# Kernel tuning notes

Hardware: AMD Instinct MI355X
Metric: run time of the kernel (lower is better)

Reference implementation:

```python
import jax, jax.numpy as jnp
import numpy as np

LN2 = float(np.log(2.0))

def ssp(v):
    # PhysNet shifted softplus activation
    return jax.nn.softplus(v) - LN2

N, F, E, K, L = 50000, 128, 800000, 64, 3

def setup_inputs() -> dict:
    key = jax.random.key(0)
    ks = jax.random.split(key, 16)
    sc = 1.0 / np.sqrt(F)
    x = jax.random.normal(ks[0], (N, F), dtype=jnp.float32)
    rbf = jax.random.uniform(ks[1], (E, K), dtype=jnp.float32)
    idx_i = jnp.sort(jax.random.randint(ks[2], (E,), 0, N, dtype=jnp.int32))
    idx_j = jax.random.randint(ks[3], (E,), 0, N, dtype=jnp.int32)
    Wk2f = jax.random.normal(ks[4], (K, F), dtype=jnp.float32) / np.sqrt(K)
    Wi = jax.random.normal(ks[5], (F, F), dtype=jnp.float32) * sc
    bi = jnp.zeros((F,), jnp.float32)
    Wj = jax.random.normal(ks[6], (F, F), dtype=jnp.float32) * sc
    bj = jnp.zeros((F,), jnp.float32)
    Wr1 = jax.random.normal(ks[7], (L, F, F), dtype=jnp.float32) * sc
    br1 = jnp.zeros((L, F), jnp.float32)
    Wr2 = jax.random.normal(ks[8], (L, F, F), dtype=jnp.float32) * sc
    br2 = jnp.zeros((L, F), jnp.float32)
    Wf = jax.random.normal(ks[9], (F, F), dtype=jnp.float32) * sc
    bf = jnp.zeros((F,), jnp.float32)
    u = jnp.ones((F,), jnp.float32)
    return dict(x=x, rbf=rbf, Wk2f=Wk2f, Wi=Wi, bi=bi, Wj=Wj, bj=bj,
                Wr1=Wr1, br1=br1, Wr2=Wr2, br2=br2, Wf=Wf, bf=bf, u=u,
                idx_i=idx_i, idx_j=idx_j)

def reference(x, rbf, Wk2f, Wi, bi, Wj, bj, Wr1, br1, Wr2, br2, Wf, bf, u, idx_i, idx_j):
    xa = ssp(x)                                   # [N,F] (drop_rate=0 -> no dropout)
    g = rbf @ Wk2f                                # [E,F] rbf gate
    xi = ssp(xa @ Wi + bi)                        # [N,F]
    xj_all = ssp(xa @ Wj + bj)                    # [N,F]
    msgs = g * xj_all[idx_j]                      # [E,F] gather + gate
    xj = jax.ops.segment_sum(msgs, idx_i, num_segments=N)  # [N,F] scatter-reduce
    m = xi + xj
    for l in range(L):                            # PhysNet residual blocks
        y = ssp(m)
        m = m + ssp(y @ Wr1[l] + br1[l]) @ Wr2[l] + br2[l]
    m = ssp(m)
    return u * x + (m @ Wf + bf)
```

## Files before the change

### kernel.cpp

```cpp
#include <hip/hip_runtime.h>
#include <hip/hip_bf16.h>
#include <math.h>

typedef unsigned short u16;
typedef short bf16x8 __attribute__((ext_vector_type(8)));
typedef float f32x4 __attribute__((ext_vector_type(4)));

#define LN2F 0.693147180559945f

__device__ __forceinline__ float bf2f(u16 h) {
  union { unsigned int i; float f; } v; v.i = ((unsigned int)h) << 16; return v.f;
}
__device__ __forceinline__ u16 f2bf(float f) {
  union { float f; unsigned int i; } v; v.f = f;
  unsigned int x = v.i;
  return (u16)((x + 0x7fffu + ((x >> 16) & 1u)) >> 16);
}
__device__ __forceinline__ float sspf(float v) {
  return fmaxf(v, 0.0f) + __logf(1.0f + __expf(-fabsf(v))) - LN2F;
}
template<int MODE>
__device__ __forceinline__ float ldv(const void* p, size_t i) {
  if constexpr (MODE == 0) return bf2f(((const u16*)p)[i]);
  else                     return ((const float*)p)[i];
}

__global__ void probe_k(const u16* __restrict__ x, int* __restrict__ flag) {
  __shared__ int sf;
  if (threadIdx.x == 0) sf = 0;
  __syncthreads();
  int f = 0;
  for (int i = threadIdx.x; i < 4096; i += 256) {
    const unsigned e = (x[i] >> 7) & 0xFFu;
    if (e >= 0xC0u) f = 1;
  }
  if (f) atomicOr(&sf, 1);
  __syncthreads();
  if (threadIdx.x == 0) *flag = sf;
}

template<int NB>
__device__ __forceinline__ void copy_lin(const u16* __restrict__ g, u16* s, int tid) {
  constexpr int CH = NB / 16;
#pragma unroll
  for (int c = tid; c < CH; c += 256)
    *(bf16x8*)(s + (size_t)c * 8) = *(const bf16x8*)(g + (size_t)c * 8);
}

__device__ __forceinline__ void wload(const u16* __restrict__ g, bf16x8* w, int tid) {
#pragma unroll
  for (int p = 0; p < 8; ++p) w[p] = *(const bf16x8*)(g + (size_t)(tid + p * 256) * 8);
  if (tid < 128) w[8] = *(const bf16x8*)(g + (size_t)(2048 + tid) * 8);
}
__device__ __forceinline__ void wstore(u16* s, const bf16x8* w, int tid) {
#pragma unroll
  for (int p = 0; p < 8; ++p) *(bf16x8*)(s + (size_t)(tid + p * 256) * 8) = w[p];
  if (tid < 128) *(bf16x8*)(s + (size_t)(2048 + tid) * 8) = w[8];
}

template<int KSTEPS, int LDW>
__device__ __forceinline__ void mm_lds(const u16* sA, const u16* sW, f32x4* acc,
                                       int m16, int quad) {
#pragma unroll
  for (int s = 0; s < KSTEPS; ++s) {
    const int k0 = s * 32 + quad * 8;
    bf16x8 a = *(const bf16x8*)(sA + (size_t)m16 * LDW + k0);
#pragma unroll
    for (int t = 0; t < 8; ++t) {
      bf16x8 b = *(const bf16x8*)(sW + (size_t)(t * 16 + m16) * LDW + k0);
      acc[t] = __builtin_amdgcn_mfma_f32_16x16x32_bf16(a, b, acc[t], 0, 0, 0);
    }
  }
}

template<int MODE>
__global__ __launch_bounds__(256) void prep_k(
    const int* __restrict__ mode,
    const void* __restrict__ Wi, const void* __restrict__ Wj,
    const void* __restrict__ Wf, const void* __restrict__ Wk2f,
    const void* __restrict__ Wr1, const void* __restrict__ Wr2,
    u16* __restrict__ WT, int L)
{
  if (*mode != MODE) return;
  const int b = blockIdx.x, tid = threadIdx.x;
  constexpr size_t esz = (MODE == 0) ? 2 : 4;
  const void* src; u16* dst; int KD = 128, LDW = 136;
  if      (b == 0) { src = Wi;  dst = WT; }
  else if (b == 1) { src = Wj;  dst = WT + 17408; }
  else if (b == 2) { src = Wf;  dst = WT + 2 * 17408; }
  else if (b == 3) { src = Wk2f; dst = WT + (size_t)(3 + 2 * L) * 17408; KD = 64; LDW = 72; }
  else if (b < 4 + L) { int l = b - 4;     src = (const char*)Wr1 + (size_t)l * 16384 * esz; dst = WT + (size_t)(3 + l) * 17408; }
  else                { int l = b - 4 - L; src = (const char*)Wr2 + (size_t)l * 16384 * esz; dst = WT + (size_t)(3 + L + l) * 17408; }

  const int n  = tid & 127;
  const int kh = (tid >> 7) * (KD >> 1);
  for (int c = 0; c < (KD >> 4); ++c) {
    const int k0 = kh + c * 8;
    bf16x8 rv;
#pragma unroll
    for (int j = 0; j < 8; ++j)
      rv[j] = (short)f2bf(ldv<MODE>(src, (size_t)(k0 + j) * 128 + n));
    *(bf16x8*)(dst + (size_t)n * LDW + k0) = rv;
  }
}

template<int MODE>
__global__ __launch_bounds__(256) void in_k(
    const int* __restrict__ mode, const void* __restrict__ x,
    const u16* __restrict__ WiT, const u16* __restrict__ WjT,
    const void* __restrict__ bi, const void* __restrict__ bj,
    float* __restrict__ mb, u16* __restrict__ xjt, int N)
{
  if (*mode != MODE) return;
  __shared__ u16 sW[128 * 136];
  const int tid = threadIdx.x, lane = tid & 63, wave = tid >> 6;
  const int m16 = lane & 15, quad = lane >> 4;
  const int row_tile = blockIdx.x * 64 + wave * 16;
  int arow = row_tile + m16; if (arow >= N) arow = N - 1;

  bf16x8 af[4];
#pragma unroll
  for (int s = 0; s < 4; ++s) {
    const int k0 = s * 32 + quad * 8;
    if constexpr (MODE == 0) {
      bf16x8 raw = *(const bf16x8*)((const u16*)x + (size_t)arow * 128 + k0);
#pragma unroll
      for (int j = 0; j < 8; ++j) af[s][j] = (short)f2bf(sspf(bf2f((u16)raw[j])));
    } else {
      const float* ap = (const float*)x + (size_t)arow * 128 + k0;
      float4 lo = *(const float4*)ap, hi = *(const float4*)(ap + 4);
      float v[8] = {lo.x, lo.y, lo.z, lo.w, hi.x, hi.y, hi.z, hi.w};
#pragma unroll
      for (int j = 0; j < 8; ++j) af[s][j] = (short)f2bf(sspf(v[j]));
    }
  }

  copy_lin<128 * 136 * 2>(WiT, sW, tid);
  __syncthreads();
  f32x4 aI[8], aJ[8];
#pragma unroll
  for (int t = 0; t < 8; ++t) aI[t] = (f32x4){0.f, 0.f, 0.f, 0.f};
  bf16x8 w[9];
  wload(WjT, w, tid);
#pragma unroll
  for (int s = 0; s < 4; ++s) {
    const int k0 = s * 32 + quad * 8;
#pragma unroll
    for (int t = 0; t < 8; ++t) {
      bf16x8 b = *(const bf16x8*)(sW + (size_t)(t * 16 + m16) * 136 + k0);
      aI[t] = __builtin_amdgcn_mfma_f32_16x16x32_bf16(af[s], b, aI[t], 0, 0, 0);
    }
  }
  __syncthreads();
  wstore(sW, w, tid);
  __syncthreads();
#pragma unroll
  for (int t = 0; t < 8; ++t) aJ[t] = (f32x4){0.f, 0.f, 0.f, 0.f};
#pragma unroll
  for (int s = 0; s < 4; ++s) {
    const int k0 = s * 32 + quad * 8;
#pragma unroll
    for (int t = 0; t < 8; ++t) {
      bf16x8 b = *(const bf16x8*)(sW + (size_t)(t * 16 + m16) * 136 + k0);
      aJ[t] = __builtin_amdgcn_mfma_f32_16x16x32_bf16(af[s], b, aJ[t], 0, 0, 0);
    }
  }

#pragma unroll
  for (int t = 0; t < 8; ++t) {
    const int col = t * 16 + m16;
    const float biv = ldv<MODE>(bi, col), bjv = ldv<MODE>(bj, col);
#pragma unroll
    for (int r = 0; r < 4; ++r) {
      const int ro = row_tile + quad * 4 + r;
      if (ro >= N) continue;
      const size_t off = (size_t)ro * 128 + col;
      mb[off]  = sspf(aI[t][r] + biv);
      xjt[off] = f2bf(sspf(aJ[t][r] + bjv));
    }
  }
}

template<int MODE>
__global__ __launch_bounds__(256) void edge_k(
    const int* __restrict__ mode,
    const void* __restrict__ rbf, const u16* __restrict__ WkT,
    const u16* __restrict__ xj_all, const int* __restrict__ idx_i,
    const int* __restrict__ idx_j, float* __restrict__ mb, int E)
{
  if (*mode != MODE) return;
  __shared__ u16 sW[128 * 72];
  __shared__ u16 sMsg[64][132];
  __shared__ int sIi[64];
  const int tid = threadIdx.x;
  const int e0 = blockIdx.x * 64;
  const int lane = tid & 63, wave = tid >> 6;
  const int m16 = lane & 15, quad = lane >> 4;
  const int lebase = wave * 16 + quad * 4;

  if (tid < 64) sIi[tid] = (e0 + tid < E) ? idx_i[e0 + tid] : -1;
  int jrow[4];
#pragma unroll
  for (int r = 0; r < 4; ++r) {
    const int e = e0 + lebase + r;
    jrow[r] = (e < E) ? idx_j[e] : 0;
  }

  bf16x8 w[5];
#pragma unroll
  for (int p = 0; p < 4; ++p) w[p] = *(const bf16x8*)(WkT + (size_t)(tid + p * 256) * 8);
  if (tid < 128) w[4] = *(const bf16x8*)(WkT + (size_t)(1024 + tid) * 8);

  int er = e0 + wave * 16 + m16; if (er >= E) er = E - 1;
  bf16x8 rbH[2]; float4 rbF[4];
  if constexpr (MODE == 0) {
    const u16* p = (const u16*)rbf + (size_t)er * 64 + quad * 8;
    rbH[0] = *(const bf16x8*)p;
    rbH[1] = *(const bf16x8*)(p + 32);
  } else {
    const float* p = (const float*)rbf + (size_t)er * 64 + quad * 8;
    rbF[0] = *(const float4*)p;        rbF[1] = *(const float4*)(p + 4);
    rbF[2] = *(const float4*)(p + 32); rbF[3] = *(const float4*)(p + 36);
  }

  u16 xg[8][4];
#pragma unroll
  for (int r = 0; r < 4; ++r) {
    const u16* xr = xj_all + (size_t)jrow[r] * 128 + m16;
#pragma unroll
    for (int t = 0; t < 8; ++t) xg[t][r] = xr[t * 16];
  }

#pragma unroll
  for (int p = 0; p < 4; ++p) *(bf16x8*)(sW + (size_t)(tid + p * 256) * 8) = w[p];
  if (tid < 128) *(bf16x8*)(sW + (size_t)(1024 + tid) * 8) = w[4];
  __syncthreads();

  f32x4 acc[8];
#pragma unroll
  for (int t = 0; t < 8; ++t) acc[t] = (f32x4){0.f, 0.f, 0.f, 0.f};
#pragma unroll
  for (int s = 0; s < 2; ++s) {
    bf16x8 af;
    if constexpr (MODE == 0) af = rbH[s];
    else {
      const float4 lo = rbF[2 * s], hi = rbF[2 * s + 1];
      af[0] = f2bf(lo.x); af[1] = f2bf(lo.y); af[2] = f2bf(lo.z); af[3] = f2bf(lo.w);
      af[4] = f2bf(hi.x); af[5] = f2bf(hi.y); af[6] = f2bf(hi.z); af[7] = f2bf(hi.w);
    }
    const int k0 = s * 32 + quad * 8;
#pragma unroll
    for (int t = 0; t < 8; ++t) {
      bf16x8 b = *(const bf16x8*)(sW + (size_t)(t * 16 + m16) * 72 + k0);
      acc[t] = __builtin_amdgcn_mfma_f32_16x16x32_bf16(af, b, acc[t], 0, 0, 0);
    }
  }

#pragma unroll
  for (int t = 0; t < 8; ++t) {
    const int col = t * 16 + m16;
#pragma unroll
    for (int r = 0; r < 4; ++r) {
      const float xvf = (e0 + lebase + r < E) ? bf2f(xg[t][r]) : 0.f;
      sMsg[lebase + r][col] = f2bf(acc[t][r] * xvf);
    }
  }
  __syncthreads();

  const int scol = tid & 127;
  const int sbeg = (tid >> 7) * 32;
  float sum = 0.f;
  int cur = sIi[sbeg];
#pragma unroll 4
  for (int r = 0; r < 32; ++r) {
    const int node = sIi[sbeg + r];
    if (node != cur) {
      if (cur >= 0) atomicAdd(&mb[(size_t)cur * 128 + scol], sum);
      sum = 0.f; cur = node;
    }
    sum += bf2f(sMsg[sbeg + r][scol]);
  }
  if (cur >= 0) atomicAdd(&mb[(size_t)cur * 128 + scol], sum);
}

template<int MODE>
__global__ __launch_bounds__(256) void resid_k(
    const int* __restrict__ mode, const float* __restrict__ mb,
    const u16* __restrict__ WT,
    const void* __restrict__ br1, const void* __restrict__ br2,
    const void* __restrict__ bfv, const void* __restrict__ x,
    const void* __restrict__ u, void* __restrict__ out, int N, int L)
{
  if (*mode != MODE) return;
  __shared__ u16 sW[128 * 136];
  __shared__ u16 sM[64 * 136];
  const int tid = threadIdx.x, lane = tid & 63, wave = tid >> 6;
  const int m16 = lane & 15, quad = lane >> 4;
  const int rbase = blockIdx.x * 64 + wave * 16 + quad * 4;
  u16* sMw = sM + (size_t)(wave * 16) * 136;

  f32x4 m[8];
#pragma unroll
  for (int t = 0; t < 8; ++t) {
    const int col = t * 16 + m16;
#pragma unroll
    for (int r = 0; r < 4; ++r) {
      int ro = rbase + r; if (ro >= N) ro = N - 1;
      m[t][r] = mb[(size_t)ro * 128 + col];
    }
  }

  const u16* W1T = WT + (size_t)3 * 17408;
  const u16* W2T = WT + (size_t)(3 + L) * 17408;
  bf16x8 w[9];

  for (int l = 0; l < L; ++l) {
    wload(W1T + (size_t)l * 17408, w, tid);
#pragma unroll
    for (int t = 0; t < 8; ++t) {
      const int col = t * 16 + m16;
#pragma unroll
      for (int r = 0; r < 4; ++r)
        sM[(size_t)(wave * 16 + quad * 4 + r) * 136 + col] = f2bf(sspf(m[t][r]));
    }
    wstore(sW, w, tid);
    __syncthreads();

    f32x4 a1[8];
#pragma unroll
    for (int t = 0; t < 8; ++t) a1[t] = (f32x4){0.f, 0.f, 0.f, 0.f};
    mm_lds<4, 136>(sMw, sW, a1, m16, quad);
    __syncthreads();

    wload(W2T + (size_t)l * 17408, w, tid);
#pragma unroll
    for (int t = 0; t < 8; ++t) {
      const int col = t * 16 + m16;
      const float b1v = ldv<MODE>(br1, (size_t)l * 128 + col);
#pragma unroll
      for (int r = 0; r < 4; ++r)
        sM[(size_t)(wave * 16 + quad * 4 + r) * 136 + col] = f2bf(sspf(a1[t][r] + b1v));
    }
    wstore(sW, w, tid);
    __syncthreads();

    mm_lds<4, 136>(sMw, sW, m, m16, quad);
#pragma unroll
    for (int t = 0; t < 8; ++t) {
      const float b2v = ldv<MODE>(br2, (size_t)l * 128 + t * 16 + m16);
#pragma unroll
      for (int r = 0; r < 4; ++r) m[t][r] += b2v;
    }
    __syncthreads();
  }

  wload(WT + (size_t)2 * 17408, w, tid);
#pragma unroll
  for (int t = 0; t < 8; ++t) {
    const int col = t * 16 + m16;
#pragma unroll
    for (int r = 0; r < 4; ++r)
      sM[(size_t)(wave * 16 + quad * 4 + r) * 136 + col] = f2bf(sspf(m[t][r]));
  }
  wstore(sW, w, tid);
  __syncthreads();

  f32x4 o[8];
#pragma unroll
  for (int t = 0; t < 8; ++t) o[t] = (f32x4){0.f, 0.f, 0.f, 0.f};
  mm_lds<4, 136>(sMw, sW, o, m16, quad);

#pragma unroll
  for (int t = 0; t < 8; ++t) {
    const int col = t * 16 + m16;
    const float bv = ldv<MODE>(bfv, col), uvv = ldv<MODE>(u, col);
#pragma unroll
    for (int r = 0; r < 4; ++r) {
      const int ro = rbase + r;
      if (ro >= N) continue;
      const size_t off = (size_t)ro * 128 + col;
      const float ov = uvv * ldv<MODE>(x, off) + o[t][r] + bv;
      if constexpr (MODE == 0) ((u16*)out)[off] = f2bf(ov);
      else                     ((float*)out)[off] = ov;
    }
  }
}

template<int MODE>
static void run_pipeline(const int* flag,
                         const void* x, const void* rbf, const void* Wk2f,
                         const void* Wi, const void* bi, const void* Wj, const void* bj,
                         const void* Wr1, const void* br1, const void* Wr2, const void* br2,
                         const void* Wf, const void* bfv, const void* uv,
                         const int* idx_i, const int* idx_j,
                         u16* WT, float* mb, u16* xjt, void* out,
                         int N, int E, int L, hipStream_t stream)
{
  const dim3 blk(256);
  const int gridN = (N + 63) / 64;
  const int gridE = (E + 63) / 64;

  prep_k<MODE><<<4 + 2 * L, blk, 0, stream>>>(flag, Wi, Wj, Wf, Wk2f, Wr1, Wr2, WT, L);
  in_k<MODE><<<gridN, blk, 0, stream>>>(flag, x, WT, WT + 17408, bi, bj, mb, xjt, N);
  edge_k<MODE><<<gridE, blk, 0, stream>>>(flag, rbf, WT + (size_t)(3 + 2 * L) * 17408,
                                          xjt, idx_i, idx_j, mb, E);
  resid_k<MODE><<<gridN, blk, 0, stream>>>(flag, mb, WT, br1, br2, bfv, x, uv, out, N, L);
}

extern "C" void kernel_launch(void* const* d_in, const int* in_sizes, int n_in,
                              void* d_out, int out_size, void* d_ws, size_t ws_size,
                              hipStream_t stream)
{
  const void* x    = d_in[0];
  const void* rbf  = d_in[1];
  const void* Wk2f = d_in[2];
  const void* Wi   = d_in[3];
  const void* bi   = d_in[4];
  const void* Wj   = d_in[5];
  const void* bj   = d_in[6];
  const void* Wr1  = d_in[7];
  const void* br1  = d_in[8];
  const void* Wr2  = d_in[9];
  const void* br2  = d_in[10];
  const void* Wf   = d_in[11];
  const void* bfv  = d_in[12];
  const void* uv   = d_in[13];
  const int* idx_i = (const int*)d_in[14];
  const int* idx_j = (const int*)d_in[15];

  const int N = in_sizes[0] / 128;
  const int E = in_sizes[14];
  const int L = in_sizes[7] / (128 * 128);

  int* flag = (int*)d_ws;
  char* wsb = (char*)d_ws + 16;
  const size_t avail = ws_size > 16 ? ws_size - 16 : 0;

  const size_t needW  = ((size_t)(3 + 2 * L) * 17408 + 9216) * 2;
  const size_t needWA = (needW + 255) & ~(size_t)255;
  u16* WT = (u16*)wsb;
  char* wsb2 = wsb + needWA;
  const size_t avail2 = (avail > needWA) ? avail - needWA : 0;

  const size_t needF = (size_t)N * 512;
  const size_t needH = (size_t)N * 256;

  float* mb0; u16* xjt0;
  if (avail2 >= needF + needH) { mb0 = (float*)wsb2; xjt0 = (u16*)(wsb2 + needF); }
  else                         { mb0 = (float*)wsb2; xjt0 = (u16*)d_out; }
  float* mb1; u16* xjt1;
  if (avail2 >= needF + needH)      { mb1 = (float*)wsb2;  xjt1 = (u16*)(wsb2 + needF); }
  else if (avail2 >= needF)         { mb1 = (float*)wsb2;  xjt1 = (u16*)d_out; }
  else                              { mb1 = (float*)d_out; xjt1 = (u16*)wsb2; }

  probe_k<<<1, 256, 0, stream>>>((const u16*)x, flag);
  run_pipeline<0>(flag, x, rbf, Wk2f, Wi, bi, Wj, bj, Wr1, br1, Wr2, br2,
                  Wf, bfv, uv, idx_i, idx_j, WT, mb0, xjt0, d_out, N, E, L, stream);
  run_pipeline<1>(flag, x, rbf, Wk2f, Wi, bi, Wj, bj, Wr1, br1, Wr2, br2,
                  Wf, bfv, uv, idx_i, idx_j, WT, mb1, xjt1, d_out, N, E, L, stream);
}
```

Baseline: 510.6 us.

## Merge dtype-specialized pipelines into runtime-branch kernels and double resid tile rows

The two templated pipelines, which launched eight kernels with half of them exiting early, are replaced by single kernels that branch on the runtime dtype flag. This removes four empty launches per call. The residual kernel now processes 128 rows per block instead of 64, so each staged weight matrix in LDS is reused across twice as many rows. In exchange it roughly doubles the accumulator registers and the LDS for the activation tile, which may lower occupancy.

New measurement: 549.7 us. 7.7% more time.

```diff
diff --git a/kernel.cpp b/kernel.cpp
--- a/kernel.cpp
+++ b/kernel.cpp
@@ -19,11 +19,6 @@
 __device__ __forceinline__ float sspf(float v) {
   return fmaxf(v, 0.0f) + __logf(1.0f + __expf(-fabsf(v))) - LN2F;
 }
-template<int MODE>
-__device__ __forceinline__ float ldv(const void* p, size_t i) {
-  if constexpr (MODE == 0) return bf2f(((const u16*)p)[i]);
-  else                     return ((const float*)p)[i];
-}
 
 __global__ void probe_k(const u16* __restrict__ x, int* __restrict__ flag) {
   __shared__ int sf;
@@ -73,7 +68,6 @@
   }
 }
 
-template<int MODE>
 __global__ __launch_bounds__(256) void prep_k(
     const int* __restrict__ mode,
     const void* __restrict__ Wi, const void* __restrict__ Wj,
@@ -81,9 +75,9 @@
     const void* __restrict__ Wr1, const void* __restrict__ Wr2,
     u16* __restrict__ WT, int L)
 {
-  if (*mode != MODE) return;
+  const int md = *mode;
   const int b = blockIdx.x, tid = threadIdx.x;
-  constexpr size_t esz = (MODE == 0) ? 2 : 4;
+  const size_t esz = md ? 4 : 2;
   const void* src; u16* dst; int KD = 128, LDW = 136;
   if      (b == 0) { src = Wi;  dst = WT; }
   else if (b == 1) { src = Wj;  dst = WT + 17408; }
@@ -94,24 +88,34 @@
 
   const int n  = tid & 127;
   const int kh = (tid >> 7) * (KD >> 1);
-  for (int c = 0; c < (KD >> 4); ++c) {
-    const int k0 = kh + c * 8;
-    bf16x8 rv;
-#pragma unroll
-    for (int j = 0; j < 8; ++j)
-      rv[j] = (short)f2bf(ldv<MODE>(src, (size_t)(k0 + j) * 128 + n));
-    *(bf16x8*)(dst + (size_t)n * LDW + k0) = rv;
-  }
-}
-
-template<int MODE>
+  if (md == 0) {
+    for (int c = 0; c < (KD >> 4); ++c) {
+      const int k0 = kh + c * 8;
+      bf16x8 rv;
+#pragma unroll
+      for (int j = 0; j < 8; ++j)
+        rv[j] = (short)((const u16*)src)[(size_t)(k0 + j) * 128 + n];
+      *(bf16x8*)(dst + (size_t)n * LDW + k0) = rv;
+    }
+  } else {
+    for (int c = 0; c < (KD >> 4); ++c) {
+      const int k0 = kh + c * 8;
+      bf16x8 rv;
+#pragma unroll
+      for (int j = 0; j < 8; ++j)
+        rv[j] = (short)f2bf(((const float*)src)[(size_t)(k0 + j) * 128 + n]);
+      *(bf16x8*)(dst + (size_t)n * LDW + k0) = rv;
+    }
+  }
+}
+
 __global__ __launch_bounds__(256) void in_k(
     const int* __restrict__ mode, const void* __restrict__ x,
     const u16* __restrict__ WiT, const u16* __restrict__ WjT,
     const void* __restrict__ bi, const void* __restrict__ bj,
     float* __restrict__ mb, u16* __restrict__ xjt, int N)
 {
-  if (*mode != MODE) return;
+  const int md = *mode;
   __shared__ u16 sW[128 * 136];
   const int tid = threadIdx.x, lane = tid & 63, wave = tid >> 6;
   const int m16 = lane & 15, quad = lane >> 4;
@@ -119,14 +123,18 @@
   int arow = row_tile + m16; if (arow >= N) arow = N - 1;
 
   bf16x8 af[4];
-#pragma unroll
-  for (int s = 0; s < 4; ++s) {
-    const int k0 = s * 32 + quad * 8;
-    if constexpr (MODE == 0) {
+  if (md == 0) {
+#pragma unroll
+    for (int s = 0; s < 4; ++s) {
+      const int k0 = s * 32 + quad * 8;
       bf16x8 raw = *(const bf16x8*)((const u16*)x + (size_t)arow * 128 + k0);
 #pragma unroll
       for (int j = 0; j < 8; ++j) af[s][j] = (short)f2bf(sspf(bf2f((u16)raw[j])));
-    } else {
+    }
+  } else {
+#pragma unroll
+    for (int s = 0; s < 4; ++s) {
+      const int k0 = s * 32 + quad * 8;
       const float* ap = (const float*)x + (size_t)arow * 128 + k0;
       float4 lo = *(const float4*)ap, hi = *(const float4*)(ap + 4);
       float v[8] = {lo.x, lo.y, lo.z, lo.w, hi.x, hi.y, hi.z, hi.w};
@@ -169,7 +177,9 @@
 #pragma unroll
   for (int t = 0; t < 8; ++t) {
     const int col = t * 16 + m16;
-    const float biv = ldv<MODE>(bi, col), bjv = ldv<MODE>(bj, col);
+    float biv, bjv;
+    if (md == 0) { biv = bf2f(((const u16*)bi)[col]); bjv = bf2f(((const u16*)bj)[col]); }
+    else         { biv = ((const float*)bi)[col];     bjv = ((const float*)bj)[col]; }
 #pragma unroll
     for (int r = 0; r < 4; ++r) {
       const int ro = row_tile + quad * 4 + r;
@@ -181,14 +191,13 @@
   }
 }
 
-template<int MODE>
 __global__ __launch_bounds__(256) void edge_k(
     const int* __restrict__ mode,
     const void* __restrict__ rbf, const u16* __restrict__ WkT,
     const u16* __restrict__ xj_all, const int* __restrict__ idx_i,
     const int* __restrict__ idx_j, float* __restrict__ mb, int E)
 {
-  if (*mode != MODE) return;
+  const int md = *mode;
   __shared__ u16 sW[128 * 72];
   __shared__ u16 sMsg[64][132];
   __shared__ int sIi[64];
@@ -212,15 +221,19 @@
   if (tid < 128) w[4] = *(const bf16x8*)(WkT + (size_t)(1024 + tid) * 8);
 
   int er = e0 + wave * 16 + m16; if (er >= E) er = E - 1;
-  bf16x8 rbH[2]; float4 rbF[4];
-  if constexpr (MODE == 0) {
+  bf16x8 rb[2];
+  if (md == 0) {
     const u16* p = (const u16*)rbf + (size_t)er * 64 + quad * 8;
-    rbH[0] = *(const bf16x8*)p;
-    rbH[1] = *(const bf16x8*)(p + 32);
+    rb[0] = *(const bf16x8*)p;
+    rb[1] = *(const bf16x8*)(p + 32);
   } else {
     const float* p = (const float*)rbf + (size_t)er * 64 + quad * 8;
-    rbF[0] = *(const float4*)p;        rbF[1] = *(const float4*)(p + 4);
-    rbF[2] = *(const float4*)(p + 32); rbF[3] = *(const float4*)(p + 36);
+    float4 a0 = *(const float4*)p,        a1 = *(const float4*)(p + 4);
+    float4 a2 = *(const float4*)(p + 32), a3 = *(const float4*)(p + 36);
+    rb[0][0] = f2bf(a0.x); rb[0][1] = f2bf(a0.y); rb[0][2] = f2bf(a0.z); rb[0][3] = f2bf(a0.w);
+    rb[0][4] = f2bf(a1.x); rb[0][5] = f2bf(a1.y); rb[0][6] = f2bf(a1.z); rb[0][7] = f2bf(a1.w);
+    rb[1][0] = f2bf(a2.x); rb[1][1] = f2bf(a2.y); rb[1][2] = f2bf(a2.z); rb[1][3] = f2bf(a2.w);
+    rb[1][4] = f2bf(a3.x); rb[1][5] = f2bf(a3.y); rb[1][6] = f2bf(a3.z); rb[1][7] = f2bf(a3.w);
   }
 
   u16 xg[8][4];
@@ -241,18 +254,11 @@
   for (int t = 0; t < 8; ++t) acc[t] = (f32x4){0.f, 0.f, 0.f, 0.f};
 #pragma unroll
   for (int s = 0; s < 2; ++s) {
-    bf16x8 af;
-    if constexpr (MODE == 0) af = rbH[s];
-    else {
-      const float4 lo = rbF[2 * s], hi = rbF[2 * s + 1];
-      af[0] = f2bf(lo.x); af[1] = f2bf(lo.y); af[2] = f2bf(lo.z); af[3] = f2bf(lo.w);
-      af[4] = f2bf(hi.x); af[5] = f2bf(hi.y); af[6] = f2bf(hi.z); af[7] = f2bf(hi.w);
-    }
     const int k0 = s * 32 + quad * 8;
 #pragma unroll
     for (int t = 0; t < 8; ++t) {
       bf16x8 b = *(const bf16x8*)(sW + (size_t)(t * 16 + m16) * 72 + k0);
-      acc[t] = __builtin_amdgcn_mfma_f32_16x16x32_bf16(af, b, acc[t], 0, 0, 0);
+      acc[t] = __builtin_amdgcn_mfma_f32_16x16x32_bf16(rb[s], b, acc[t], 0, 0, 0);
     }
   }
 
@@ -283,7 +289,6 @@
   if (cur >= 0) atomicAdd(&mb[(size_t)cur * 128 + scol], sum);
 }
 
-template<int MODE>
 __global__ __launch_bounds__(256) void resid_k(
     const int* __restrict__ mode, const float* __restrict__ mb,
     const u16* __restrict__ WT,
@@ -291,22 +296,25 @@
     const void* __restrict__ bfv, const void* __restrict__ x,
     const void* __restrict__ u, void* __restrict__ out, int N, int L)
 {
-  if (*mode != MODE) return;
+  const int md = *mode;
   __shared__ u16 sW[128 * 136];
-  __shared__ u16 sM[64 * 136];
+  __shared__ u16 sM[128 * 136];
   const int tid = threadIdx.x, lane = tid & 63, wave = tid >> 6;
   const int m16 = lane & 15, quad = lane >> 4;
-  const int rbase = blockIdx.x * 64 + wave * 16 + quad * 4;
-  u16* sMw = sM + (size_t)(wave * 16) * 136;
-
-  f32x4 m[8];
-#pragma unroll
-  for (int t = 0; t < 8; ++t) {
-    const int col = t * 16 + m16;
-#pragma unroll
-    for (int r = 0; r < 4; ++r) {
-      int ro = rbase + r; if (ro >= N) ro = N - 1;
-      m[t][r] = mb[(size_t)ro * 128 + col];
+  const int rb0 = blockIdx.x * 128;
+
+  f32x4 m[2][8];
+#pragma unroll
+  for (int s = 0; s < 2; ++s) {
+#pragma unroll
+    for (int t = 0; t < 8; ++t) {
+      const int col = t * 16 + m16;
+#pragma unroll
+      for (int r = 0; r < 4; ++r) {
+        int ro = rb0 + s * 64 + wave * 16 + quad * 4 + r;
+        if (ro >= N) ro = N - 1;
+        m[s][t][r] = mb[(size_t)ro * 128 + col];
+      }
     }
   }
 
@@ -317,94 +325,96 @@
   for (int l = 0; l < L; ++l) {
     wload(W1T + (size_t)l * 17408, w, tid);
 #pragma unroll
-    for (int t = 0; t < 8; ++t) {
-      const int col = t * 16 + m16;
-#pragma unroll
-      for (int r = 0; r < 4; ++r)
-        sM[(size_t)(wave * 16 + quad * 4 + r) * 136 + col] = f2bf(sspf(m[t][r]));
-    }
+    for (int s = 0; s < 2; ++s)
+#pragma unroll
+      for (int t = 0; t < 8; ++t) {
+        const int col = t * 16 + m16;
+#pragma unroll
+        for (int r = 0; r < 4; ++r)
+          sM[(size_t)(s * 64 + wave * 16 + quad * 4 + r) * 136 + col] = f2bf(sspf(m[s][t][r]));
+      }
     wstore(sW, w, tid);
     __syncthreads();
 
-    f32x4 a1[8];
-#pragma unroll
-    for (int t = 0; t < 8; ++t) a1[t] = (f32x4){0.f, 0.f, 0.f, 0.f};
-    mm_lds<4, 136>(sMw, sW, a1, m16, quad);
+    f32x4 a1[2][8];
+#pragma unroll
+    for (int s = 0; s < 2; ++s) {
+#pragma unroll
+      for (int t = 0; t < 8; ++t) a1[s][t] = (f32x4){0.f, 0.f, 0.f, 0.f};
+      mm_lds<4, 136>(sM + (size_t)(s * 64 + wave * 16) * 136, sW, a1[s], m16, quad);
+    }
     __syncthreads();
 
     wload(W2T + (size_t)l * 17408, w, tid);
 #pragma unroll
-    for (int t = 0; t < 8; ++t) {
-      const int col = t * 16 + m16;
-      const float b1v = ldv<MODE>(br1, (size_t)l * 128 + col);
-#pragma unroll
-      for (int r = 0; r < 4; ++r)
-        sM[(size_t)(wave * 16 + quad * 4 + r) * 136 + col] = f2bf(sspf(a1[t][r] + b1v));
-    }
+    for (int s = 0; s < 2; ++s)
+#pragma unroll
+      for (int t = 0; t < 8; ++t) {
+        const int col = t * 16 + m16;
+        float b1v;
+        if (md == 0) b1v = bf2f(((const u16*)br1)[(size_t)l * 128 + col]);
+        else         b1v = ((const float*)br1)[(size_t)l * 128 + col];
+#pragma unroll
+        for (int r = 0; r < 4; ++r)
+          sM[(size_t)(s * 64 + wave * 16 + quad * 4 + r) * 136 + col] = f2bf(sspf(a1[s][t][r] + b1v));
+      }
     wstore(sW, w, tid);
     __syncthreads();
 
-    mm_lds<4, 136>(sMw, sW, m, m16, quad);
-#pragma unroll
-    for (int t = 0; t < 8; ++t) {
-      const float b2v = ldv<MODE>(br2, (size_t)l * 128 + t * 16 + m16);
-#pragma unroll
-      for (int r = 0; r < 4; ++r) m[t][r] += b2v;
+#pragma unroll
+    for (int s = 0; s < 2; ++s)
+      mm_lds<4, 136>(sM + (size_t)(s * 64 + wave * 16) * 136, sW, m[s], m16, quad);
+#pragma unroll
+    for (int t = 0; t < 8; ++t) {
+      float b2v;
+      if (md == 0) b2v = bf2f(((const u16*)br2)[(size_t)l * 128 + t * 16 + m16]);
+      else         b2v = ((const float*)br2)[(size_t)l * 128 + t * 16 + m16];
+#pragma unroll
+      for (int s = 0; s < 2; ++s)
+#pragma unroll
+        for (int r = 0; r < 4; ++r) m[s][t][r] += b2v;
     }
     __syncthreads();
   }
 
   wload(WT + (size_t)2 * 17408, w, tid);
+#pragma unroll
+  for (int s = 0; s < 2; ++s)
+#pragma unroll
+    for (int t = 0; t < 8; ++t) {
+      const int col = t * 16 + m16;
+#pragma unroll
+      for (int r = 0; r < 4; ++r)
+        sM[(size_t)(s * 64 + wave * 16 + quad * 4 + r) * 136 + col] = f2bf(sspf(m[s][t][r]));
+    }
+  wstore(sW, w, tid);
+  __syncthreads();
+
+  f32x4 o[2][8];
+#pragma unroll
+  for (int s = 0; s < 2; ++s) {
+#pragma unroll
+    for (int t = 0; t < 8; ++t) o[s][t] = (f32x4){0.f, 0.f, 0.f, 0.f};
+    mm_lds<4, 136>(sM + (size_t)(s * 64 + wave * 16) * 136, sW, o[s], m16, quad);
+  }
+
 #pragma unroll
   for (int t = 0; t < 8; ++t) {
     const int col = t * 16 + m16;
-#pragma unroll
-    for (int r = 0; r < 4; ++r)
-      sM[(size_t)(wave * 16 + quad * 4 + r) * 136 + col] = f2bf(sspf(m[t][r]));
-  }
-  wstore(sW, w, tid);
-  __syncthreads();
-
-  f32x4 o[8];
-#pragma unroll
-  for (int t = 0; t < 8; ++t) o[t] = (f32x4){0.f, 0.f, 0.f, 0.f};
-  mm_lds<4, 136>(sMw, sW, o, m16, quad);
-
-#pragma unroll
-  for (int t = 0; t < 8; ++t) {
-    const int col = t * 16 + m16;
-    const float bv = ldv<MODE>(bfv, col), uvv = ldv<MODE>(u, col);
-#pragma unroll
-    for (int r = 0; r < 4; ++r) {
-      const int ro = rbase + r;
-      if (ro >= N) continue;
-      const size_t off = (size_t)ro * 128 + col;
-      const float ov = uvv * ldv<MODE>(x, off) + o[t][r] + bv;
-      if constexpr (MODE == 0) ((u16*)out)[off] = f2bf(ov);
-      else                     ((float*)out)[off] = ov;
-    }
-  }
-}
-
-template<int MODE>
-static void run_pipeline(const int* flag,
-                         const void* x, const void* rbf, const void* Wk2f,
-                         const void* Wi, const void* bi, const void* Wj, const void* bj,
-                         const void* Wr1, const void* br1, const void* Wr2, const void* br2,
-                         const void* Wf, const void* bfv, const void* uv,
-                         const int* idx_i, const int* idx_j,
-                         u16* WT, float* mb, u16* xjt, void* out,
-                         int N, int E, int L, hipStream_t stream)
-{
-  const dim3 blk(256);
-  const int gridN = (N + 63) / 64;
-  const int gridE = (E + 63) / 64;
-
-  prep_k<MODE><<<4 + 2 * L, blk, 0, stream>>>(flag, Wi, Wj, Wf, Wk2f, Wr1, Wr2, WT, L);
-  in_k<MODE><<<gridN, blk, 0, stream>>>(flag, x, WT, WT + 17408, bi, bj, mb, xjt, N);
-  edge_k<MODE><<<gridE, blk, 0, stream>>>(flag, rbf, WT + (size_t)(3 + 2 * L) * 17408,
-                                          xjt, idx_i, idx_j, mb, E);
-  resid_k<MODE><<<gridN, blk, 0, stream>>>(flag, mb, WT, br1, br2, bfv, x, uv, out, N, L);
+    float bv, uvv;
+    if (md == 0) { bv = bf2f(((const u16*)bfv)[col]); uvv = bf2f(((const u16*)u)[col]); }
+    else         { bv = ((const float*)bfv)[col];     uvv = ((const float*)u)[col]; }
+#pragma unroll
+    for (int s = 0; s < 2; ++s)
+#pragma unroll
+      for (int r = 0; r < 4; ++r) {
+        const int ro = rb0 + s * 64 + wave * 16 + quad * 4 + r;
+        if (ro >= N) continue;
+        const size_t off = (size_t)ro * 128 + col;
+        if (md == 0) ((u16*)out)[off]  = f2bf(uvv * bf2f(((const u16*)x)[off]) + o[s][t][r] + bv);
+        else         ((float*)out)[off] = uvv * ((const float*)x)[off] + o[s][t][r] + bv;
+      }
+  }
 }
 
 extern "C" void kernel_launch(void* const* d_in, const int* in_sizes, int n_in,
@@ -445,17 +455,20 @@
   const size_t needF = (size_t)N * 512;
   const size_t needH = (size_t)N * 256;
 
-  float* mb0; u16* xjt0;
-  if (avail2 >= needF + needH) { mb0 = (float*)wsb2; xjt0 = (u16*)(wsb2 + needF); }
-  else                         { mb0 = (float*)wsb2; xjt0 = (u16*)d_out; }
-  float* mb1; u16* xjt1;
-  if (avail2 >= needF + needH)      { mb1 = (float*)wsb2;  xjt1 = (u16*)(wsb2 + needF); }
-  else if (avail2 >= needF)         { mb1 = (float*)wsb2;  xjt1 = (u16*)d_out; }
-  else                              { mb1 = (float*)d_out; xjt1 = (u16*)wsb2; }
+  float* mb; u16* xjt;
+  if (avail2 >= needF + needH) { mb = (float*)wsb2; xjt = (u16*)(wsb2 + needF); }
+  else if (avail2 >= needF)    { mb = (float*)wsb2; xjt = (u16*)d_out; }
+  else                         { mb = (float*)d_out; xjt = (u16*)wsb2; }
+
+  const dim3 blk(256);
+  const int gridN = (N + 63) / 64;
+  const int gridR = (N + 127) / 128;
+  const int gridE = (E + 63) / 64;
 
   probe_k<<<1, 256, 0, stream>>>((const u16*)x, flag);
-  run_pipeline<0>(flag, x, rbf, Wk2f, Wi, bi, Wj, bj, Wr1, br1, Wr2, br2,
-                  Wf, bfv, uv, idx_i, idx_j, WT, mb0, xjt0, d_out, N, E, L, stream);
-  run_pipeline<1>(flag, x, rbf, Wk2f, Wi, bi, Wj, bj, Wr1, br1, Wr2, br2,
-                  Wf, bfv, uv, idx_i, idx_j, WT, mb1, xjt1, d_out, N, E, L, stream);
-}
+  prep_k<<<4 + 2 * L, blk, 0, stream>>>(flag, Wi, Wj, Wf, Wk2f, Wr1, Wr2, WT, L);
+  in_k<<<gridN, blk, 0, stream>>>(flag, x, WT, WT + 17408, bi, bj, mb, xjt, N);
+  edge_k<<<gridE, blk, 0, stream>>>(flag, rbf, WT + (size_t)(3 + 2 * L) * 17408,
+                                    xjt, idx_i, idx_j, mb, E);
+  resid_k<<<gridR, blk, 0, stream>>>(flag, mb, WT, br1, br2, bfv, x, uv, d_out, N, L);
+}
```
